# Kernel tuning notes

Measured on AMD Instinct MI355X. Metric: run time of the kernel, lower is better.

Reference implementation:

```python
import jax, jax.numpy as jnp
import numpy as np

N_NODES = 100000
N_EDGES = 1600000
D_IN = 128
D_HID = 128
N_LAYERS = 3


def setup_inputs() -> dict:
    key = jax.random.key(0)
    ks = jax.random.split(key, 7)
    x = jax.random.normal(ks[0], (N_NODES, D_IN), dtype=jnp.float32)
    edge_index = jax.random.randint(ks[1], (2, N_EDGES), 0, N_NODES, dtype=jnp.int32)
    s = 1.0 / np.sqrt(D_HID)
    # stacked per-layer MLP params: lin1 (in->h), lin2 (h->h); in==h==128 for all layers
    W1 = jax.random.uniform(ks[2], (N_LAYERS, D_IN, D_HID), jnp.float32, -s, s)
    b1 = jax.random.uniform(ks[3], (N_LAYERS, D_HID), jnp.float32, -s, s)
    W2 = jax.random.uniform(ks[4], (N_LAYERS, D_HID, D_HID), jnp.float32, -s, s)
    b2 = jax.random.uniform(ks[5], (N_LAYERS, D_HID), jnp.float32, -s, s)
    return {"x": x, "edge_index": edge_index, "W1": W1, "b1": b1, "W2": W2, "b2": b2}


def _gin_layer(x, src, dst, W1, b1, W2, b2):
    # GINConv: out = MLP((1+eps)*x + sum_{j in N(i)} x_j), eps = 0
    agg = jax.ops.segment_sum(x[src], dst, num_segments=N_NODES)  # [N, C]
    h = x + agg
    h = jnp.maximum(h @ W1 + b1, 0.0)  # MLP internal ReLU
    return h @ W2 + b2


def reference(x, edge_index, W1, b1, W2, b2):
    src, dst = edge_index[0], edge_index[1]
    for i in range(N_LAYERS):
        x = _gin_layer(x, src, dst, W1[i], b1[i], W2[i], b2[i])
        if i < N_LAYERS - 1:  # inter-layer act (norm=Identity, dropout=0)
            x = jnp.maximum(x, 0.0)
    return x
```

## Files before the change

kernel.cpp:

```cpp
#include <hip/hip_runtime.h>
#include <hip/hip_bf16.h>

#define D 128

typedef float f32x4 __attribute__((ext_vector_type(4)));
typedef __bf16 bf16x8 __attribute__((ext_vector_type(8)));

__device__ __forceinline__ unsigned short f2bf(float f) {
  unsigned int u = __float_as_uint(f);
  u += 0x7fff + ((u >> 16) & 1);
  return (unsigned short)(u >> 16);
}

__device__ __forceinline__ void gl_lds16(const void* g, void* l) {
  __builtin_amdgcn_global_load_lds(
      (const __attribute__((address_space(1))) unsigned int*)g,
      (__attribute__((address_space(3))) unsigned int*)l, 16, 0, 0);
}

__device__ __forceinline__ int wave_incl_scan(int v, int lane) {
#pragma unroll
  for (int d = 1; d < 64; d <<= 1) {
    int t = __shfl_up(v, d);
    if (lane >= d) v += t;
  }
  return v;
}

#define NBK 196
#define CHUNK 4096

__global__ __launch_bounds__(256) void k_bhist(const int* __restrict__ dst, int E,
                                               int* __restrict__ bcount) {
  __shared__ int cnt[NBK];
  const int tid = threadIdx.x;
  for (int i = tid; i < NBK; i += 256) cnt[i] = 0;
  __syncthreads();
  const int e0 = blockIdx.x * CHUNK;
  const int emax = min(e0 + CHUNK, E);
  for (int e = e0 + tid; e < emax; e += 256)
    atomicAdd(&cnt[((unsigned)dst[e]) >> 9], 1);
  __syncthreads();
  for (int i = tid; i < NBK; i += 256)
    if (cnt[i]) atomicAdd(&bcount[i], cnt[i]);
}

__global__ __launch_bounds__(256) void k_binA(const int* __restrict__ src,
                                              const int* __restrict__ dst, int E,
                                              const int* __restrict__ bcount,
                                              int* __restrict__ bcursor,
                                              int* __restrict__ pairbuf) {
  __shared__ int cnt[NBK];
  __shared__ int base[NBK];
  __shared__ int bb[NBK];
  __shared__ int ws4[4];
  const int tid = threadIdx.x;
  const int e0 = blockIdx.x * CHUNK;
  const int emax = min(e0 + CHUNK, E);
  for (int i = tid; i < NBK; i += 256) cnt[i] = 0;
  {
    int lane = tid & 63, w = tid >> 6;
    int v = (tid < NBK) ? bcount[tid] : 0;
    int s = wave_incl_scan(v, lane);
    if (lane == 63) ws4[w] = s;
    __syncthreads();
    if (tid < NBK) {
      int off = 0;
      for (int k = 0; k < w; k++) off += ws4[k];
      bb[tid] = off + s - v;
    }
  }
  __syncthreads();
  for (int e = e0 + tid; e < emax; e += 256)
    atomicAdd(&cnt[((unsigned)dst[e]) >> 9], 1);
  __syncthreads();
  for (int i = tid; i < NBK; i += 256) {
    int c = cnt[i];
    int b = 0;
    if (c) b = atomicAdd(&bcursor[i], c) + bb[i];
    base[i] = b;
    cnt[i] = 0;
  }
  __syncthreads();
  for (int e = e0 + tid; e < emax; e += 256) {
    int d = dst[e];
    int bk = ((unsigned)d) >> 9;
    int pos = base[bk] + atomicAdd(&cnt[bk], 1);
    pairbuf[pos] = (src[e] << 9) | (d & 511);
  }
}

#define SEG_CAP 12800
__global__ __launch_bounds__(256) void k_binB(const int* __restrict__ pairbuf,
                                              const int* __restrict__ bcount,
                                              int* __restrict__ col,
                                              int* __restrict__ row_ptr, int N) {
  __shared__ int sdeg[512];
  __shared__ int rpl[512];
  __shared__ int cur[512];
  __shared__ int wsum[4];
  __shared__ int wsum2[4];
  __shared__ int stage[SEG_CAP];
  const int tid = threadIdx.x;
  const int lane = tid & 63, wid = tid >> 6;
  const int node0 = blockIdx.x << 9;
  const int nn = min(512, N - node0);
  {
    int vv = (tid < (int)blockIdx.x) ? bcount[tid] : 0;
    vv += __shfl_down(vv, 32); vv += __shfl_down(vv, 16);
    vv += __shfl_down(vv, 8);  vv += __shfl_down(vv, 4);
    vv += __shfl_down(vv, 2);  vv += __shfl_down(vv, 1);
    if (lane == 0) wsum2[wid] = vv;
  }
  for (int i = tid; i < 512; i += 256) { sdeg[i] = 0; cur[i] = 0; }
  __syncthreads();
  const int start = wsum2[0] + wsum2[1] + wsum2[2] + wsum2[3];
  const int end = start + bcount[blockIdx.x];
  const int sz = end - start;
  for (int i = tid; i < sz; i += 256)
    atomicAdd(&sdeg[pairbuf[start + i] & 511], 1);
  __syncthreads();
  int a = sdeg[2 * tid], b = sdeg[2 * tid + 1];
  int v = a + b;
  int s = wave_incl_scan(v, lane);
  if (lane == 63) wsum[wid] = s;
  __syncthreads();
  int off = 0;
  for (int k = 0; k < wid; k++) off += wsum[k];
  int e0l = off + s - v;
  rpl[2 * tid] = e0l;
  rpl[2 * tid + 1] = e0l + a;
  __syncthreads();
  for (int i = tid; i < nn; i += 256) row_ptr[node0 + i] = start + rpl[i];
  if (blockIdx.x == gridDim.x - 1 && tid == 0) row_ptr[N] = end;
  for (int i = tid; i < sz; i += 256) {
    int pk = pairbuf[start + i];
    int d = pk & 511;
    int pos = rpl[d] + atomicAdd(&cur[d], 1);
    if (pos < SEG_CAP) stage[pos] = (int)(((unsigned)pk) >> 9);
  }
  __syncthreads();
  for (int i = tid; i < sz; i += 256) col[start + i] = stage[i];
}

__global__ void k_prep(const float* __restrict__ W1, const float* __restrict__ W2,
                       unsigned short* __restrict__ Wt, int* __restrict__ bcount) {
  int b = blockIdx.x;
  if (b < 6) {
    const float* W = (b & 1) ? (W2 + (size_t)(b >> 1) * D * D) : (W1 + (size_t)(b >> 1) * D * D);
    unsigned short* O = Wt + (size_t)b * D * D;
    for (int i = threadIdx.x; i < D * D; i += 256) {
      int n = i >> 7, k = i & 127;
      O[n * D + k] = f2bf(W[k * D + n]);
    }
  } else {
    for (int i = threadIdx.x; i < 512; i += 256) bcount[i] = 0;
  }
}

__global__ __launch_bounds__(256) void k_agg(const unsigned short* __restrict__ Y,
                                             const int* __restrict__ row_ptr,
                                             const int* __restrict__ col,
                                             const float* __restrict__ bias,
                                             unsigned short* __restrict__ H, int N) {
  int wid = (blockIdx.x * 256 + threadIdx.x) >> 6;
  int lane = threadIdx.x & 63;
  if (wid >= N) return;
  const unsigned int* Yu = (const unsigned int*)Y;
  unsigned int sv = Yu[(size_t)wid * 64 + lane];
  float2 bv = ((const float2*)bias)[lane];
  float ax = bv.x + __uint_as_float(sv << 16);
  float ay = bv.y + __uint_as_float(sv & 0xffff0000u);
  int rs = row_ptr[wid], re = row_ptr[wid + 1];
  int deg = re - rs;
  int dcap = min(deg, 64);
  int cv = (lane < dcap) ? col[rs + lane] : 0;
  int j = 0;
  for (; j + 8 <= dcap; j += 8) {
    int s0 = __shfl(cv, j + 0), s1 = __shfl(cv, j + 1);
    int s2 = __shfl(cv, j + 2), s3 = __shfl(cv, j + 3);
    int s4 = __shfl(cv, j + 4), s5 = __shfl(cv, j + 5);
    int s6 = __shfl(cv, j + 6), s7 = __shfl(cv, j + 7);
    unsigned int v0 = Yu[(size_t)s0 * 64 + lane];
    unsigned int v1 = Yu[(size_t)s1 * 64 + lane];
    unsigned int v2 = Yu[(size_t)s2 * 64 + lane];
    unsigned int v3 = Yu[(size_t)s3 * 64 + lane];
    unsigned int v4 = Yu[(size_t)s4 * 64 + lane];
    unsigned int v5 = Yu[(size_t)s5 * 64 + lane];
    unsigned int v6 = Yu[(size_t)s6 * 64 + lane];
    unsigned int v7 = Yu[(size_t)s7 * 64 + lane];
    ax += ((__uint_as_float(v0 << 16) + __uint_as_float(v1 << 16)) +
           (__uint_as_float(v2 << 16) + __uint_as_float(v3 << 16))) +
          ((__uint_as_float(v4 << 16) + __uint_as_float(v5 << 16)) +
           (__uint_as_float(v6 << 16) + __uint_as_float(v7 << 16)));
    ay += ((__uint_as_float(v0 & 0xffff0000u) + __uint_as_float(v1 & 0xffff0000u)) +
           (__uint_as_float(v2 & 0xffff0000u) + __uint_as_float(v3 & 0xffff0000u))) +
          ((__uint_as_float(v4 & 0xffff0000u) + __uint_as_float(v5 & 0xffff0000u)) +
           (__uint_as_float(v6 & 0xffff0000u) + __uint_as_float(v7 & 0xffff0000u)));
  }
  for (; j < dcap; j++) {
    int s = __shfl(cv, j);
    unsigned int v = Yu[(size_t)s * 64 + lane];
    ax += __uint_as_float(v << 16);
    ay += __uint_as_float(v & 0xffff0000u);
  }
  for (int t = rs + 64; t < re; t++) {
    unsigned int v = Yu[(size_t)col[t] * 64 + lane];
    ax += __uint_as_float(v << 16);
    ay += __uint_as_float(v & 0xffff0000u);
  }
  ax = fmaxf(ax, 0.f);
  ay = fmaxf(ay, 0.f);
  unsigned int packed = ((unsigned int)f2bf(ay) << 16) | f2bf(ax);
  ((unsigned int*)H)[(size_t)wid * 64 + lane] = packed;
}

template <bool A_FP32, bool OUT_FP32>
__global__ __launch_bounds__(256) void k_gemm(const void* __restrict__ Ain,
                                              const unsigned short* __restrict__ Wt,
                                              const float* __restrict__ bias,
                                              void* __restrict__ Cout, int M, int relu) {
  __shared__ __align__(16) unsigned short As[64 * 128];
  __shared__ __align__(16) unsigned short Bs[128 * 128];
  const int tid = threadIdx.x;
  const int wid = tid >> 6, lane = tid & 63;
  const int R0 = blockIdx.x * 64;

#pragma unroll
  for (int g = 0; g < 8; g++) {
    int flat = g * 256 + tid;
    int n = flat >> 4, p = flat & 15;
    int l = p ^ (n & 15);
    gl_lds16(Wt + (size_t)n * D + l * 8, &Bs[(size_t)(g * 256 + wid * 64) * 8]);
  }
  if (A_FP32) {
    const float* A = (const float*)Ain;
#pragma unroll
    for (int g = 0; g < 4; g++) {
      int flat = g * 256 + tid;
      int row = flat >> 4, p = flat & 15;
      int l = p ^ (row & 15);
      float4 a0 = make_float4(0.f, 0.f, 0.f, 0.f), a1 = a0;
      if (R0 + row < M) {
        a0 = *(const float4*)(A + (size_t)(R0 + row) * D + l * 8);
        a1 = *(const float4*)(A + (size_t)(R0 + row) * D + l * 8 + 4);
      }
      ushort4 v0, v1;
      v0.x = f2bf(a0.x); v0.y = f2bf(a0.y); v0.z = f2bf(a0.z); v0.w = f2bf(a0.w);
      v1.x = f2bf(a1.x); v1.y = f2bf(a1.y); v1.z = f2bf(a1.z); v1.w = f2bf(a1.w);
      *(ushort4*)&As[row * D + p * 8] = v0;
      *(ushort4*)&As[row * D + p * 8 + 4] = v1;
    }
  } else {
    const unsigned short* A = (const unsigned short*)Ain;
#pragma unroll
    for (int g = 0; g < 4; g++) {
      int flat = g * 256 + tid;
      int row = flat >> 4, p = flat & 15;
      int l = p ^ (row & 15);
      gl_lds16(A + (size_t)(R0 + row) * D + l * 8, &As[(size_t)(g * 256 + wid * 64) * 8]);
    }
  }
  __syncthreads();

  const int wr = wid >> 1, wc = wid & 1;
  const int lm = lane & 15, lq = lane >> 4;
  f32x4 acc[2][4];
#pragma unroll
  for (int i = 0; i < 2; i++)
#pragma unroll
    for (int j = 0; j < 4; j++) acc[i][j] = f32x4{0.f, 0.f, 0.f, 0.f};

#pragma unroll
  for (int kc = 0; kc < 4; kc++) {
    const int pc = (kc * 4 + lq) ^ lm;
    bf16x8 af[2], bfr[4];
#pragma unroll
    for (int i = 0; i < 2; i++)
      af[i] = *(const bf16x8*)&As[(wr * 32 + i * 16 + lm) * D + pc * 8];
#pragma unroll
    for (int j = 0; j < 4; j++)
      bfr[j] = *(const bf16x8*)&Bs[(wc * 64 + j * 16 + lm) * D + pc * 8];
#pragma unroll
    for (int i = 0; i < 2; i++)
#pragma unroll
      for (int j = 0; j < 4; j++)
        acc[i][j] = __builtin_amdgcn_mfma_f32_16x16x32_bf16(af[i], bfr[j], acc[i][j], 0, 0, 0);
  }

  float bv[4];
#pragma unroll
  for (int j = 0; j < 4; j++) bv[j] = bias ? bias[wc * 64 + j * 16 + lm] : 0.f;
#pragma unroll
  for (int i = 0; i < 2; i++) {
#pragma unroll
    for (int reg = 0; reg < 4; reg++) {
      const int gr = R0 + wr * 32 + i * 16 + lq * 4 + reg;
      if (gr < M) {
#pragma unroll
        for (int j = 0; j < 4; j++) {
          const int gc = wc * 64 + j * 16 + lm;
          float v = acc[i][j][reg] + bv[j];
          if (relu) v = fmaxf(v, 0.f);
          if (OUT_FP32)
            ((float*)Cout)[(size_t)gr * D + gc] = v;
          else
            ((unsigned short*)Cout)[(size_t)gr * D + gc] = f2bf(v);
        }
      }
    }
  }
}

__global__ __launch_bounds__(256) void k_gemm2(const unsigned short* __restrict__ Ain,
                                               const unsigned short* __restrict__ W2t,
                                               const unsigned short* __restrict__ W1t,
                                               const float* __restrict__ b2,
                                               unsigned short* __restrict__ Cout, int M) {
  __shared__ __align__(16) unsigned short As[64 * 128];
  __shared__ __align__(16) unsigned short Bs[128 * 128];
  const int tid = threadIdx.x;
  const int wid = tid >> 6, lane = tid & 63;
  const int R0 = blockIdx.x * 64;

#pragma unroll
  for (int g = 0; g < 8; g++) {
    int flat = g * 256 + tid;
    int n = flat >> 4, p = flat & 15;
    int l = p ^ (n & 15);
    gl_lds16(W2t + (size_t)n * D + l * 8, &Bs[(size_t)(g * 256 + wid * 64) * 8]);
  }
#pragma unroll
  for (int g = 0; g < 4; g++) {
    int flat = g * 256 + tid;
    int row = flat >> 4, p = flat & 15;
    int l = p ^ (row & 15);
    gl_lds16(Ain + (size_t)(R0 + row) * D + l * 8, &As[(size_t)(g * 256 + wid * 64) * 8]);
  }
  __syncthreads();

  const int wr = wid >> 1, wc = wid & 1;
  const int lm = lane & 15, lq = lane >> 4;
  f32x4 acc[2][4];
#pragma unroll
  for (int i = 0; i < 2; i++)
#pragma unroll
    for (int j = 0; j < 4; j++) acc[i][j] = f32x4{0.f, 0.f, 0.f, 0.f};
#pragma unroll
  for (int kc = 0; kc < 4; kc++) {
    const int pc = (kc * 4 + lq) ^ lm;
    bf16x8 af[2], bfr[4];
#pragma unroll
    for (int i = 0; i < 2; i++)
      af[i] = *(const bf16x8*)&As[(wr * 32 + i * 16 + lm) * D + pc * 8];
#pragma unroll
    for (int j = 0; j < 4; j++)
      bfr[j] = *(const bf16x8*)&Bs[(wc * 64 + j * 16 + lm) * D + pc * 8];
#pragma unroll
    for (int i = 0; i < 2; i++)
#pragma unroll
      for (int j = 0; j < 4; j++)
        acc[i][j] = __builtin_amdgcn_mfma_f32_16x16x32_bf16(af[i], bfr[j], acc[i][j], 0, 0, 0);
  }
  __syncthreads();

#pragma unroll
  for (int g = 0; g < 8; g++) {
    int flat = g * 256 + tid;
    int n = flat >> 4, p = flat & 15;
    int l = p ^ (n & 15);
    gl_lds16(W1t + (size_t)n * D + l * 8, &Bs[(size_t)(g * 256 + wid * 64) * 8]);
  }
  {
    float bv[4];
#pragma unroll
    for (int j = 0; j < 4; j++) bv[j] = b2[wc * 64 + j * 16 + lm];
#pragma unroll
    for (int i = 0; i < 2; i++) {
#pragma unroll
      for (int reg = 0; reg < 4; reg++) {
        const int row = wr * 32 + i * 16 + lq * 4 + reg;
#pragma unroll
        for (int j = 0; j < 4; j++) {
          const int gc = wc * 64 + j * 16 + lm;
          float v = fmaxf(acc[i][j][reg] + bv[j], 0.f);
          As[row * D + (((gc >> 3) ^ (row & 15)) << 3) + (gc & 7)] = f2bf(v);
        }
      }
    }
  }
  __syncthreads();

  f32x4 acc2[2][4];
#pragma unroll
  for (int i = 0; i < 2; i++)
#pragma unroll
    for (int j = 0; j < 4; j++) acc2[i][j] = f32x4{0.f, 0.f, 0.f, 0.f};
#pragma unroll
  for (int kc = 0; kc < 4; kc++) {
    const int pc = (kc * 4 + lq) ^ lm;
    bf16x8 af[2], bfr[4];
#pragma unroll
    for (int i = 0; i < 2; i++)
      af[i] = *(const bf16x8*)&As[(wr * 32 + i * 16 + lm) * D + pc * 8];
#pragma unroll
    for (int j = 0; j < 4; j++)
      bfr[j] = *(const bf16x8*)&Bs[(wc * 64 + j * 16 + lm) * D + pc * 8];
#pragma unroll
    for (int i = 0; i < 2; i++)
#pragma unroll
      for (int j = 0; j < 4; j++)
        acc2[i][j] = __builtin_amdgcn_mfma_f32_16x16x32_bf16(af[i], bfr[j], acc2[i][j], 0, 0, 0);
  }
#pragma unroll
  for (int i = 0; i < 2; i++) {
#pragma unroll
    for (int reg = 0; reg < 4; reg++) {
      const int gr = R0 + wr * 32 + i * 16 + lq * 4 + reg;
      if (gr < M) {
#pragma unroll
        for (int j = 0; j < 4; j++) {
          const int gc = wc * 64 + j * 16 + lm;
          Cout[(size_t)gr * D + gc] = f2bf(acc2[i][j][reg]);
        }
      }
    }
  }
}

extern "C" void kernel_launch(void* const* d_in, const int* in_sizes, int n_in,
                              void* d_out, int out_size, void* d_ws, size_t ws_size,
                              hipStream_t stream) {
  const float* x  = (const float*)d_in[0];
  const int*   ei = (const int*)d_in[1];
  const float* W1 = (const float*)d_in[2];
  const float* b1 = (const float*)d_in[3];
  const float* W2 = (const float*)d_in[4];
  const float* b2 = (const float*)d_in[5];
  const int N = in_sizes[0] / D;
  const int E = in_sizes[1] / 2;
  const int* src = ei;
  const int* dst = ei + E;

  char* ws = (char*)d_ws;
  unsigned short* Wt   = (unsigned short*)ws;
  unsigned short* bufA = Wt + 6 * D * D;
  unsigned short* bufB = bufA + (size_t)(N + 1) * D;
  int* pairbuf = (int*)bufB;
  int* row_ptr = (int*)(bufB + (size_t)(N + 1) * D);
  int* colv    = row_ptr + (N + 1);
  int* bcount  = colv + E;
  int* bcursor = bcount + 256;
  float* OUT   = (float*)d_out;

  const int CB = (E + CHUNK - 1) / CHUNK;
  const int GB = (N + 63) / 64;
  const int AB = (N + 3) / 4;
  const int BKB = (N + 511) / 512;

  k_prep<<<7, 256, 0, stream>>>(W1, W2, Wt, bcount);
  k_bhist<<<CB, 256, 0, stream>>>(dst, E, bcount);
  k_binA<<<CB, 256, 0, stream>>>(src, dst, E, bcount, bcursor, pairbuf);
  k_binB<<<BKB, 256, 0, stream>>>(pairbuf, bcount, colv, row_ptr, N);

  k_gemm<true, false><<<GB, 256, 0, stream>>>(x, Wt + 0 * D * D, nullptr, bufA, N, 0);
  k_agg<<<AB, 256, 0, stream>>>(bufA, row_ptr, colv, b1, bufB, N);
  k_gemm2<<<GB, 256, 0, stream>>>(bufB, Wt + 1 * D * D, Wt + 2 * D * D, b2, bufA, N);
  k_agg<<<AB, 256, 0, stream>>>(bufA, row_ptr, colv, b1 + D, bufB, N);
  k_gemm2<<<GB, 256, 0, stream>>>(bufB, Wt + 3 * D * D, Wt + 4 * D * D, b2 + D, bufA, N);
  k_agg<<<AB, 256, 0, stream>>>(bufA, row_ptr, colv, b1 + 2 * D, bufB, N);
  k_gemm<false, true><<<GB, 256, 0, stream>>>(bufB, Wt + 5 * D * D, b2 + 2 * D, OUT, N, 0);
  (void)n_in; (void)out_size; (void)ws_size;
}
```

Before: 420.6 us.

## Fuse GEMM and aggregation stages into persistent cooperative megakernel with grid barriers

Replaces the seven per-stage launches (GEMM, aggregation, fused MLP GEMM) with one persistent cooperative kernel that loops over row tiles and nodes and separates stages with a software grid barrier. Weight staging is split into 64-column halves to cut shared memory and allow 5 blocks per CU. This targets launch overhead and inter-kernel tail gaps, but adds barrier spin costs, reloads weights per tile, and the grid size is capped by the occupancy query. A fallback to the old launch sequence is kept.

```diff
diff --git a/kernel.cpp b/kernel.cpp
--- a/kernel.cpp
+++ b/kernel.cpp
@@ -2,6 +2,7 @@
 #include <hip/hip_bf16.h>
 
 #define D 128
+#define DD (128 * 128)
 
 typedef float f32x4 __attribute__((ext_vector_type(4)));
 typedef __bf16 bf16x8 __attribute__((ext_vector_type(8)));
@@ -147,14 +148,248 @@
                        unsigned short* __restrict__ Wt, int* __restrict__ bcount) {
   int b = blockIdx.x;
   if (b < 6) {
-    const float* W = (b & 1) ? (W2 + (size_t)(b >> 1) * D * D) : (W1 + (size_t)(b >> 1) * D * D);
-    unsigned short* O = Wt + (size_t)b * D * D;
-    for (int i = threadIdx.x; i < D * D; i += 256) {
+    const float* W = (b & 1) ? (W2 + (size_t)(b >> 1) * DD) : (W1 + (size_t)(b >> 1) * DD);
+    unsigned short* O = Wt + (size_t)b * DD;
+    for (int i = threadIdx.x; i < DD; i += 256) {
       int n = i >> 7, k = i & 127;
       O[n * D + k] = f2bf(W[k * D + n]);
     }
   } else {
-    for (int i = threadIdx.x; i < 512; i += 256) bcount[i] = 0;
+    for (int i = threadIdx.x; i < 516; i += 256) bcount[i] = 0;
+  }
+}
+
+__device__ __forceinline__ void gsync(int* cnt, int* gen) {
+  __syncthreads();
+  if (threadIdx.x == 0) {
+    int g = __hip_atomic_load(gen, __ATOMIC_RELAXED, __HIP_MEMORY_SCOPE_AGENT);
+    __threadfence();
+    if (__hip_atomic_fetch_add(cnt, 1, __ATOMIC_ACQ_REL, __HIP_MEMORY_SCOPE_AGENT) ==
+        (int)gridDim.x - 1) {
+      __hip_atomic_store(cnt, 0, __ATOMIC_RELAXED, __HIP_MEMORY_SCOPE_AGENT);
+      __hip_atomic_fetch_add(gen, 1, __ATOMIC_RELEASE, __HIP_MEMORY_SCOPE_AGENT);
+    } else {
+      while (__hip_atomic_load(gen, __ATOMIC_ACQUIRE, __HIP_MEMORY_SCOPE_AGENT) == g)
+        __builtin_amdgcn_s_sleep(2);
+    }
+    __threadfence();
+  }
+  __syncthreads();
+}
+
+__device__ __forceinline__ void stage_w_half(const unsigned short* __restrict__ W, int n0,
+                                             unsigned short* Bs, int tid) {
+#pragma unroll
+  for (int g = 0; g < 4; g++) {
+    int flat = g * 256 + tid;
+    int n = flat >> 4, p = flat & 15, l = p ^ (n & 15);
+    gl_lds16(W + (size_t)(n0 + n) * D + l * 8, &Bs[(size_t)(g * 256 + (tid >> 6) * 64) * 8]);
+  }
+}
+
+__device__ __forceinline__ void stage_a_bf(const unsigned short* __restrict__ A, int R0,
+                                           unsigned short* As, int tid) {
+#pragma unroll
+  for (int g = 0; g < 4; g++) {
+    int flat = g * 256 + tid;
+    int row = flat >> 4, p = flat & 15, l = p ^ (row & 15);
+    gl_lds16(A + (size_t)(R0 + row) * D + l * 8,
+             &As[(size_t)(g * 256 + (tid >> 6) * 64) * 8]);
+  }
+}
+
+__device__ __forceinline__ void mma_half(const unsigned short* As, const unsigned short* Bs,
+                                         int wid, int lm, int lq, f32x4 a[4]) {
+#pragma unroll
+  for (int kc = 0; kc < 4; kc++) {
+    const int pc = (kc * 4 + lq) ^ lm;
+    bf16x8 af = *(const bf16x8*)&As[(wid * 16 + lm) * D + pc * 8];
+#pragma unroll
+    for (int j = 0; j < 4; j++) {
+      bf16x8 bf = *(const bf16x8*)&Bs[(j * 16 + lm) * D + pc * 8];
+      a[j] = __builtin_amdgcn_mfma_f32_16x16x32_bf16(af, bf, a[j], 0, 0, 0);
+    }
+  }
+}
+
+__global__ __launch_bounds__(256, 5) void k_mega(
+    const float* __restrict__ x, unsigned short* __restrict__ bufA,
+    unsigned short* __restrict__ bufB, const int* __restrict__ row_ptr,
+    const int* __restrict__ col, const unsigned short* __restrict__ Wt,
+    const float* __restrict__ b1, const float* __restrict__ b2,
+    float* __restrict__ OUT, int N, int* __restrict__ bar) {
+  __shared__ __align__(16) unsigned short As[64 * D];
+  __shared__ __align__(16) unsigned short Bs[64 * D];
+  const int tid = threadIdx.x, wid = tid >> 6, lane = tid & 63;
+  const int lm = lane & 15, lq = lane >> 4;
+  const int nT = (N + 63) >> 6;
+  int* cnt = bar;
+  int* gen = bar + 1;
+
+  for (int t = blockIdx.x; t < nT; t += gridDim.x) {
+    const int R0 = t << 6;
+#pragma unroll
+    for (int g = 0; g < 4; g++) {
+      int flat = g * 256 + tid, row = flat >> 4, p = flat & 15, l = p ^ (row & 15);
+      float4 q0 = make_float4(0.f, 0.f, 0.f, 0.f), q1 = q0;
+      if (R0 + row < N) {
+        q0 = *(const float4*)(x + (size_t)(R0 + row) * D + l * 8);
+        q1 = *(const float4*)(x + (size_t)(R0 + row) * D + l * 8 + 4);
+      }
+      ushort4 v0, v1;
+      v0.x = f2bf(q0.x); v0.y = f2bf(q0.y); v0.z = f2bf(q0.z); v0.w = f2bf(q0.w);
+      v1.x = f2bf(q1.x); v1.y = f2bf(q1.y); v1.z = f2bf(q1.z); v1.w = f2bf(q1.w);
+      *(ushort4*)&As[row * D + p * 8] = v0;
+      *(ushort4*)&As[row * D + p * 8 + 4] = v1;
+    }
+#pragma unroll
+    for (int h = 0; h < 2; h++) {
+      stage_w_half(Wt, h * 64, Bs, tid);
+      __syncthreads();
+      f32x4 a[4];
+#pragma unroll
+      for (int j = 0; j < 4; j++) a[j] = f32x4{0.f, 0.f, 0.f, 0.f};
+      mma_half(As, Bs, wid, lm, lq, a);
+#pragma unroll
+      for (int j = 0; j < 4; j++)
+#pragma unroll
+        for (int r = 0; r < 4; r++) {
+          int gr = R0 + wid * 16 + lq * 4 + r;
+          if (gr < N) bufA[(size_t)gr * D + h * 64 + j * 16 + lm] = f2bf(a[j][r]);
+        }
+      __syncthreads();
+    }
+  }
+  gsync(cnt, gen);
+
+#pragma unroll 1
+  for (int L = 0; L < 3; L++) {
+    {
+      const unsigned int* Yu = (const unsigned int*)bufA;
+      unsigned int* Hu = (unsigned int*)bufB;
+      const float2 bv = ((const float2*)(b1 + (size_t)L * D))[lane];
+      const int nw = gridDim.x << 2;
+      for (int node = (blockIdx.x << 2) + wid; node < N; node += nw) {
+        unsigned int sv = Yu[(size_t)node * 64 + lane];
+        float ax = bv.x + __uint_as_float(sv << 16);
+        float ay = bv.y + __uint_as_float(sv & 0xffff0000u);
+        int rs = row_ptr[node], re = row_ptr[node + 1];
+        int dcap = min(re - rs, 64);
+        int cv = (lane < dcap) ? col[rs + lane] : 0;
+        int j = 0;
+        for (; j + 8 <= dcap; j += 8) {
+          int s0 = __shfl(cv, j + 0), s1 = __shfl(cv, j + 1);
+          int s2 = __shfl(cv, j + 2), s3 = __shfl(cv, j + 3);
+          int s4 = __shfl(cv, j + 4), s5 = __shfl(cv, j + 5);
+          int s6 = __shfl(cv, j + 6), s7 = __shfl(cv, j + 7);
+          unsigned int v0 = Yu[(size_t)s0 * 64 + lane];
+          unsigned int v1 = Yu[(size_t)s1 * 64 + lane];
+          unsigned int v2 = Yu[(size_t)s2 * 64 + lane];
+          unsigned int v3 = Yu[(size_t)s3 * 64 + lane];
+          unsigned int v4 = Yu[(size_t)s4 * 64 + lane];
+          unsigned int v5 = Yu[(size_t)s5 * 64 + lane];
+          unsigned int v6 = Yu[(size_t)s6 * 64 + lane];
+          unsigned int v7 = Yu[(size_t)s7 * 64 + lane];
+          ax += ((__uint_as_float(v0 << 16) + __uint_as_float(v1 << 16)) +
+                 (__uint_as_float(v2 << 16) + __uint_as_float(v3 << 16))) +
+                ((__uint_as_float(v4 << 16) + __uint_as_float(v5 << 16)) +
+                 (__uint_as_float(v6 << 16) + __uint_as_float(v7 << 16)));
+          ay += ((__uint_as_float(v0 & 0xffff0000u) + __uint_as_float(v1 & 0xffff0000u)) +
+                 (__uint_as_float(v2 & 0xffff0000u) + __uint_as_float(v3 & 0xffff0000u))) +
+                ((__uint_as_float(v4 & 0xffff0000u) + __uint_as_float(v5 & 0xffff0000u)) +
+                 (__uint_as_float(v6 & 0xffff0000u) + __uint_as_float(v7 & 0xffff0000u)));
+        }
+        for (; j < dcap; j++) {
+          int s = __shfl(cv, j);
+          unsigned int v = Yu[(size_t)s * 64 + lane];
+          ax += __uint_as_float(v << 16);
+          ay += __uint_as_float(v & 0xffff0000u);
+        }
+        for (int t2 = rs + 64; t2 < re; t2++) {
+          unsigned int v = Yu[(size_t)col[t2] * 64 + lane];
+          ax += __uint_as_float(v << 16);
+          ay += __uint_as_float(v & 0xffff0000u);
+        }
+        Hu[(size_t)node * 64 + lane] =
+            ((unsigned int)f2bf(fmaxf(ay, 0.f)) << 16) | f2bf(fmaxf(ax, 0.f));
+      }
+    }
+    gsync(cnt, gen);
+
+    if (L < 2) {
+      const unsigned short* Wa = Wt + (size_t)(2 * L + 1) * DD;
+      const unsigned short* Wb = Wt + (size_t)(2 * L + 2) * DD;
+      const float* bb = b2 + (size_t)L * D;
+      for (int t = blockIdx.x; t < nT; t += gridDim.x) {
+        const int R0 = t << 6;
+        stage_a_bf(bufB, R0, As, tid);
+        f32x4 acc[2][4];
+#pragma unroll
+        for (int h = 0; h < 2; h++) {
+          stage_w_half(Wa, h * 64, Bs, tid);
+          __syncthreads();
+#pragma unroll
+          for (int j = 0; j < 4; j++) acc[h][j] = f32x4{0.f, 0.f, 0.f, 0.f};
+          mma_half(As, Bs, wid, lm, lq, acc[h]);
+          __syncthreads();
+        }
+#pragma unroll
+        for (int h = 0; h < 2; h++)
+#pragma unroll
+          for (int j = 0; j < 4; j++)
+#pragma unroll
+            for (int r = 0; r < 4; r++) {
+              int row = wid * 16 + lq * 4 + r;
+              int gc = h * 64 + j * 16 + lm;
+              float v = fmaxf(acc[h][j][r] + bb[gc], 0.f);
+              As[row * D + (((gc >> 3) ^ (row & 15)) << 3) + (gc & 7)] = f2bf(v);
+            }
+        __syncthreads();
+#pragma unroll
+        for (int h = 0; h < 2; h++) {
+          stage_w_half(Wb, h * 64, Bs, tid);
+          __syncthreads();
+          f32x4 c[4];
+#pragma unroll
+          for (int j = 0; j < 4; j++) c[j] = f32x4{0.f, 0.f, 0.f, 0.f};
+          mma_half(As, Bs, wid, lm, lq, c);
+#pragma unroll
+          for (int j = 0; j < 4; j++)
+#pragma unroll
+            for (int r = 0; r < 4; r++) {
+              int gr = R0 + wid * 16 + lq * 4 + r;
+              if (gr < N) bufA[(size_t)gr * D + h * 64 + j * 16 + lm] = f2bf(c[j][r]);
+            }
+          __syncthreads();
+        }
+      }
+      gsync(cnt, gen);
+    } else {
+      const unsigned short* Wa = Wt + (size_t)5 * DD;
+      const float* bb = b2 + (size_t)2 * D;
+      for (int t = blockIdx.x; t < nT; t += gridDim.x) {
+        const int R0 = t << 6;
+        stage_a_bf(bufB, R0, As, tid);
+#pragma unroll
+        for (int h = 0; h < 2; h++) {
+          stage_w_half(Wa, h * 64, Bs, tid);
+          __syncthreads();
+          f32x4 c[4];
+#pragma unroll
+          for (int j = 0; j < 4; j++) c[j] = f32x4{0.f, 0.f, 0.f, 0.f};
+          mma_half(As, Bs, wid, lm, lq, c);
+#pragma unroll
+          for (int j = 0; j < 4; j++)
+#pragma unroll
+            for (int r = 0; r < 4; r++) {
+              int gr = R0 + wid * 16 + lq * 4 + r;
+              if (gr < N)
+                OUT[(size_t)gr * D + h * 64 + j * 16 + lm] = c[j][r] + bb[h * 64 + j * 16 + lm];
+            }
+          __syncthreads();
+        }
+      }
+    }
   }
 }
 
@@ -172,8 +407,7 @@
   float ax = bv.x + __uint_as_float(sv << 16);
   float ay = bv.y + __uint_as_float(sv & 0xffff0000u);
   int rs = row_ptr[wid], re = row_ptr[wid + 1];
-  int deg = re - rs;
-  int dcap = min(deg, 64);
+  int dcap = min(re - rs, 64);
   int cv = (lane < dcap) ? col[rs + lane] : 0;
   int j = 0;
   for (; j + 8 <= dcap; j += 8) {
@@ -211,8 +445,8 @@
   }
   ax = fmaxf(ax, 0.f);
   ay = fmaxf(ay, 0.f);
-  unsigned int packed = ((unsigned int)f2bf(ay) << 16) | f2bf(ax);
-  ((unsigned int*)H)[(size_t)wid * 64 + lane] = packed;
+  ((unsigned int*)H)[(size_t)wid * 64 + lane] =
+      ((unsigned int)f2bf(ay) << 16) | f2bf(ax);
 }
 
 template <bool A_FP32, bool OUT_FP32>
@@ -225,7 +459,6 @@
   const int tid = threadIdx.x;
   const int wid = tid >> 6, lane = tid & 63;
   const int R0 = blockIdx.x * 64;
-
 #pragma unroll
   for (int g = 0; g < 8; g++) {
     int flat = g * 256 + tid;
@@ -262,7 +495,6 @@
     }
   }
   __syncthreads();
-
   const int wr = wid >> 1, wc = wid & 1;
   const int lm = lane & 15, lq = lane >> 4;
   f32x4 acc[2][4];
@@ -270,7 +502,6 @@
   for (int i = 0; i < 2; i++)
 #pragma unroll
     for (int j = 0; j < 4; j++) acc[i][j] = f32x4{0.f, 0.f, 0.f, 0.f};
-
 #pragma unroll
   for (int kc = 0; kc < 4; kc++) {
     const int pc = (kc * 4 + lq) ^ lm;
@@ -287,7 +518,6 @@
       for (int j = 0; j < 4; j++)
         acc[i][j] = __builtin_amdgcn_mfma_f32_16x16x32_bf16(af[i], bfr[j], acc[i][j], 0, 0, 0);
   }
-
   float bv[4];
 #pragma unroll
   for (int j = 0; j < 4; j++) bv[j] = bias ? bias[wc * 64 + j * 16 + lm] : 0.f;
@@ -322,7 +552,6 @@
   const int tid = threadIdx.x;
   const int wid = tid >> 6, lane = tid & 63;
   const int R0 = blockIdx.x * 64;
-
 #pragma unroll
   for (int g = 0; g < 8; g++) {
     int flat = g * 256 + tid;
@@ -338,7 +567,6 @@
     gl_lds16(Ain + (size_t)(R0 + row) * D + l * 8, &As[(size_t)(g * 256 + wid * 64) * 8]);
   }
   __syncthreads();
-
   const int wr = wid >> 1, wc = wid & 1;
   const int lm = lane & 15, lq = lane >> 4;
   f32x4 acc[2][4];
@@ -363,7 +591,6 @@
         acc[i][j] = __builtin_amdgcn_mfma_f32_16x16x32_bf16(af[i], bfr[j], acc[i][j], 0, 0, 0);
   }
   __syncthreads();
-
 #pragma unroll
   for (int g = 0; g < 8; g++) {
     int flat = g * 256 + tid;
@@ -390,7 +617,6 @@
     }
   }
   __syncthreads();
-
   f32x4 acc2[2][4];
 #pragma unroll
   for (int i = 0; i < 2; i++)
@@ -444,13 +670,14 @@
 
   char* ws = (char*)d_ws;
   unsigned short* Wt   = (unsigned short*)ws;
-  unsigned short* bufA = Wt + 6 * D * D;
+  unsigned short* bufA = Wt + 6 * DD;
   unsigned short* bufB = bufA + (size_t)(N + 1) * D;
   int* pairbuf = (int*)bufB;
   int* row_ptr = (int*)(bufB + (size_t)(N + 1) * D);
   int* colv    = row_ptr + (N + 1);
   int* bcount  = colv + E;
   int* bcursor = bcount + 256;
+  int* bar     = bcount + 512;
   float* OUT   = (float*)d_out;
 
   const int CB = (E + CHUNK - 1) / CHUNK;
@@ -463,12 +690,27 @@
   k_binA<<<CB, 256, 0, stream>>>(src, dst, E, bcount, bcursor, pairbuf);
   k_binB<<<BKB, 256, 0, stream>>>(pairbuf, bcount, colv, row_ptr, N);
 
-  k_gemm<true, false><<<GB, 256, 0, stream>>>(x, Wt + 0 * D * D, nullptr, bufA, N, 0);
-  k_agg<<<AB, 256, 0, stream>>>(bufA, row_ptr, colv, b1, bufB, N);
-  k_gemm2<<<GB, 256, 0, stream>>>(bufB, Wt + 1 * D * D, Wt + 2 * D * D, b2, bufA, N);
-  k_agg<<<AB, 256, 0, stream>>>(bufA, row_ptr, colv, b1 + D, bufB, N);
-  k_gemm2<<<GB, 256, 0, stream>>>(bufB, Wt + 3 * D * D, Wt + 4 * D * D, b2 + D, bufA, N);
-  k_agg<<<AB, 256, 0, stream>>>(bufA, row_ptr, colv, b1 + 2 * D, bufB, N);
-  k_gemm<false, true><<<GB, 256, 0, stream>>>(bufB, Wt + 5 * D * D, b2 + 2 * D, OUT, N, 0);
+  bool mega_ok = false;
+  int nb = 0;
+  hipError_t qe = hipOccupancyMaxActiveBlocksPerMultiprocessor(&nb, k_mega, 256, 0);
+  if (qe == hipSuccess && nb >= 4) {
+    int Nv = N;
+    const int grid = (nb < 5 ? nb : 5) * 256;
+    void* args[] = {(void*)&x,  (void*)&bufA, (void*)&bufB, (void*)&row_ptr,
+                    (void*)&colv, (void*)&Wt, (void*)&b1,   (void*)&b2,
+                    (void*)&OUT, (void*)&Nv,  (void*)&bar};
+    hipError_t ce = hipLaunchCooperativeKernel(k_mega, dim3(grid), dim3(256), args, 0, stream);
+    mega_ok = (ce == hipSuccess);
+    if (!mega_ok) (void)hipGetLastError();
+  }
+  if (!mega_ok) {
+    k_gemm<true, false><<<GB, 256, 0, stream>>>(x, Wt + 0 * DD, nullptr, bufA, N, 0);
+    k_agg<<<AB, 256, 0, stream>>>(bufA, row_ptr, colv, b1, bufB, N);
+    k_gemm2<<<GB, 256, 0, stream>>>(bufB, Wt + 1 * DD, Wt + 2 * DD, b2, bufA, N);
+    k_agg<<<AB, 256, 0, stream>>>(bufA, row_ptr, colv, b1 + D, bufB, N);
+    k_gemm2<<<GB, 256, 0, stream>>>(bufB, Wt + 3 * DD, Wt + 4 * DD, b2 + D, bufA, N);
+    k_agg<<<AB, 256, 0, stream>>>(bufA, row_ptr, colv, b1 + 2 * D, bufB, N);
+    k_gemm<false, true><<<GB, 256, 0, stream>>>(bufB, Wt + 5 * DD, b2 + 2 * D, OUT, N, 0);
+  }
   (void)n_in; (void)out_size; (void)ws_size;
 }
```

After: 417.9 us. No clear change (-0.6%).
